# Kernel tuning notes

Hardware: AMD Instinct MI355X
Metric: run time of the kernel (lower is better)

Reference implementation:

```python
import jax, jax.numpy as jnp
import numpy as np

HID = 32
R = 3
B = 2
IN = 64
N = 100000
E = 1600000
G = 256


def setup_inputs() -> dict:
    key = jax.random.key(0)
    ks = jax.random.split(key, 16)
    x = jax.random.normal(ks[0], (N, IN), dtype=jnp.float32)
    src = jax.random.randint(ks[1], (E,), 0, N)
    dst = jax.random.randint(ks[2], (E,), 0, N)
    etype = jax.random.randint(ks[3], (E,), 0, R)
    graph_ids = jnp.sort(jax.random.randint(ks[4], (N,), 0, G))
    s = 0.05
    basis1 = jax.random.normal(ks[5], (B, IN, HID), dtype=jnp.float32) * s   # layer 1 basis
    basis_r = jax.random.normal(ks[6], (3, B, HID, HID), dtype=jnp.float32) * s  # layers 2-4
    w_comp = jax.random.normal(ks[7], (4, R, B), dtype=jnp.float32) * s     # per-layer basis coeffs
    loop1 = jax.random.normal(ks[8], (IN, HID), dtype=jnp.float32) * s
    loop_r = jax.random.normal(ks[9], (3, HID, HID), dtype=jnp.float32) * s
    bias = jnp.zeros((4, HID), dtype=jnp.float32)
    lin1_w = jax.random.normal(ks[10], (4 * HID, 64), dtype=jnp.float32) * s
    lin1_b = jnp.zeros((64,), dtype=jnp.float32)
    lin2_w = jax.random.normal(ks[11], (64, 1), dtype=jnp.float32) * s
    lin2_b = jnp.zeros((1,), dtype=jnp.float32)
    return dict(x=x, basis1=basis1, basis_r=basis_r, w_comp=w_comp, loop1=loop1,
                loop_r=loop_r, bias=bias, lin1_w=lin1_w, lin1_b=lin1_b,
                lin2_w=lin2_w, lin2_b=lin2_b, src=src, dst=dst, etype=etype,
                graph_ids=graph_ids, num_graphs=G)


def _rel_conv(h, basis, comp, loop_w, b, src, dst, etype, n_nodes):
    # basis-decomposed relation weights: W[r] = sum_b comp[r,b] * basis[b]
    W = jnp.einsum('rb,bio->rio', comp, basis)            # [R, in, out]
    h_rel = jnp.einsum('ni,rio->rno', h, W)               # [R, N, out]
    msg = h_rel[etype, src]                               # [E, out] edge-typed gather
    agg = jax.ops.segment_sum(msg, dst, num_segments=n_nodes)
    return agg + h @ loop_w + b                           # self-loop + bias


def reference(x, basis1, basis_r, w_comp, loop1, loop_r, bias,
              lin1_w, lin1_b, lin2_w, lin2_b,
              src, dst, etype, graph_ids, num_graphs):
    n = x.shape[0]
    h = jnp.tanh(_rel_conv(x, basis1, w_comp[0], loop1, bias[0], src, dst, etype, n))
    states = [h]
    for i in range(3):
        h = jnp.tanh(_rel_conv(h, basis_r[i], w_comp[i + 1], loop_r[i], bias[i + 1],
                               src, dst, etype, n))
        states.append(h)
    feat = jnp.concatenate(states, axis=1)                # [N, 128]
    # mean-pool nodes per graph (diff_pooling ~ dgl mean_nodes)
    summed = jax.ops.segment_sum(feat, graph_ids, num_segments=num_graphs)
    counts = jax.ops.segment_sum(jnp.ones((n,), feat.dtype), graph_ids,
                                 num_segments=num_graphs)
    pooled = summed / jnp.maximum(counts, 1.0)[:, None]   # [G, 128]
    hdn = jax.nn.relu(pooled @ lin1_w + lin1_b)
    out = jax.nn.sigmoid(hdn @ lin2_w + lin2_b)
    return out[:, 0]
```

## Files before the change

### kernel.cpp

```cpp
#include <hip/hip_runtime.h>
#include <cstdint>
#include <cmath>

#define DLO_BITS 7
#define DLO_MASK 127

__global__ __launch_bounds__(256) void prep_w1(
    const float* __restrict__ basis1,
    const float* __restrict__ w_comp,
    float* __restrict__ W1)
{
    int tid = blockIdx.x * 256 + threadIdx.x;
    if (tid < 6144) {
        int r = tid / 2048, io = tid % 2048;
        W1[tid] = w_comp[r*2] * basis1[io] + w_comp[r*2+1] * basis1[2048 + io];
    }
}

__global__ __launch_bounds__(256) void count_kernel(
    const int* __restrict__ dst, int* __restrict__ bcnt, int E, int NB)
{
    __shared__ int cnt[1024];
    for (int i = threadIdx.x; i < NB; i += 256) cnt[i] = 0;
    __syncthreads();
    int base = blockIdx.x * 4096;
    #pragma unroll
    for (int i = 0; i < 16; ++i) {
        int e = base + i * 256 + threadIdx.x;
        if (e < E) atomicAdd(&cnt[dst[e] >> DLO_BITS], 1);
    }
    __syncthreads();
    for (int i = threadIdx.x; i < NB; i += 256)
        if (cnt[i]) atomicAdd(&bcnt[i], cnt[i]);
}

__global__ __launch_bounds__(1024) void scan_kernel(
    const int* __restrict__ bcnt, int* __restrict__ bbase,
    int* __restrict__ bcur, int NB)
{
    __shared__ int s[1024];
    int t = threadIdx.x;
    int v = (t < NB) ? bcnt[t] : 0;
    s[t] = v; __syncthreads();
    for (int off = 1; off < 1024; off <<= 1) {
        int u = (t >= off) ? s[t - off] : 0;
        __syncthreads();
        s[t] += u;
        __syncthreads();
    }
    if (t < NB) { int b = s[t] - v; bbase[t] = b; bcur[t] = b; }
}

__global__ __launch_bounds__(256) void bscatter_kernel(
    const int* __restrict__ src, const int* __restrict__ dst,
    const int* __restrict__ et, int* __restrict__ bcur,
    unsigned* __restrict__ eidx1, int E, int NB)
{
    __shared__ int cnt[1024];
    __shared__ int bbs[1024];
    int tid = threadIdx.x;
    for (int i = tid; i < NB; i += 256) cnt[i] = 0;
    __syncthreads();
    int base = blockIdx.x * 8192;
    int lim = E - base; if (lim > 8192) lim = 8192;
    for (int i = tid; i < lim; i += 256)
        atomicAdd(&cnt[dst[base + i] >> DLO_BITS], 1);
    __syncthreads();
    for (int i = tid; i < NB; i += 256) {
        int c = cnt[i];
        bbs[i] = c ? atomicAdd(&bcur[i], c) : 0;
    }
    __syncthreads();
    for (int i = tid; i < NB; i += 256) cnt[i] = 0;
    __syncthreads();
    for (int i = tid; i < lim; i += 256) {
        int e = base + i;
        int d = dst[e];
        int bk = d >> DLO_BITS;
        int p = bbs[bk] + atomicAdd(&cnt[bk], 1);
        eidx1[p] = (unsigned)src[e] | ((unsigned)et[e] << 17)
                 | ((unsigned)(d & DLO_MASK) << 19);
    }
}

__global__ __launch_bounds__(256) void bucket_sort_kernel(
    const unsigned* __restrict__ eidx1, const int* __restrict__ bbase,
    const int* __restrict__ bcnt, unsigned* __restrict__ eidx2,
    int* __restrict__ row_ptr, int* __restrict__ deg, int N)
{
    __shared__ int c128[128], excl[128], w[128];
    int tid = threadIdx.x, b = blockIdx.x;
    int gbase = bbase[b], cnt = bcnt[b], n0 = b << DLO_BITS;
    if (tid < 128) c128[tid] = 0;
    __syncthreads();
    for (int k = tid; k < cnt; k += 256)
        atomicAdd(&c128[(eidx1[gbase + k] >> 19) & DLO_MASK], 1);
    __syncthreads();
    if (tid < 128) w[tid] = c128[tid];
    __syncthreads();
    for (int off = 1; off < 128; off <<= 1) {
        int u = (tid < 128 && tid >= off) ? w[tid - off] : 0;
        __syncthreads();
        if (tid < 128) w[tid] += u;
        __syncthreads();
    }
    if (tid < 128) {
        excl[tid] = w[tid] - c128[tid];
        int n = n0 + tid;
        if (n < N) { row_ptr[n] = gbase + excl[tid]; deg[n] = c128[tid]; }
        c128[tid] = 0;
    }
    __syncthreads();
    for (int k = tid; k < cnt; k += 256) {
        unsigned pk = eidx1[gbase + k];
        int dlo = (pk >> 19) & DLO_MASK;
        int p = excl[dlo] + atomicAdd(&c128[dlo], 1);
        eidx2[gbase + p] = pk;
    }
}

__global__ __launch_bounds__(256) void dense_kernel(
    const float* __restrict__ x,
    const float* __restrict__ Wrel,
    const float* __restrict__ Wloop,
    const float* __restrict__ bias_l,
    float* __restrict__ hrel,
    float* __restrict__ agg,
    int N)
{
    __shared__ float sW[4 * 2048];
    __shared__ float sH[64 * 68];
    const int tid = threadIdx.x;
    for (int i = tid; i < 3 * 2048; i += 256) sW[i] = Wrel[i];
    for (int i = tid; i < 2048; i += 256) sW[6144 + i] = Wloop[i];
    const int nb = blockIdx.x * 64;
    for (int idx = tid; idx < 64 * 64; idx += 256) {
        int n = idx >> 6, i = idx & 63;
        int gn = nb + n;
        sH[n * 68 + i] = (gn < N) ? x[(size_t)gn * 64 + i] : 0.0f;
    }
    __syncthreads();

    const int m  = tid >> 6;
    const int l  = tid & 63;
    const int ow = l & 7;
    const int ng = l >> 3;

    float acc[8][4];
    #pragma unroll
    for (int j = 0; j < 8; ++j)
        #pragma unroll
        for (int k = 0; k < 4; ++k) acc[j][k] = 0.0f;

    const float* wb = &sW[m * 2048 + ow * 4];
    #pragma unroll 2
    for (int i = 0; i < 64; i += 4) {
        float4 wv0 = *(const float4*)(wb + (i + 0) * 32);
        float4 wv1 = *(const float4*)(wb + (i + 1) * 32);
        float4 wv2 = *(const float4*)(wb + (i + 2) * 32);
        float4 wv3 = *(const float4*)(wb + (i + 3) * 32);
        #pragma unroll
        for (int j = 0; j < 8; ++j) {
            float4 hv = *(const float4*)&sH[(j * 8 + ng) * 68 + i];
            acc[j][0] += hv.x * wv0.x + hv.y * wv1.x + hv.z * wv2.x + hv.w * wv3.x;
            acc[j][1] += hv.x * wv0.y + hv.y * wv1.y + hv.z * wv2.y + hv.w * wv3.y;
            acc[j][2] += hv.x * wv0.z + hv.y * wv1.z + hv.z * wv2.z + hv.w * wv3.z;
            acc[j][3] += hv.x * wv0.w + hv.y * wv1.w + hv.z * wv2.w + hv.w * wv3.w;
        }
    }

    if (m < 3) {
        #pragma unroll
        for (int j = 0; j < 8; ++j) {
            int n = nb + j * 8 + ng;
            if (n < N)
                *(float4*)&hrel[((size_t)m * N + n) * 32 + ow * 4] =
                    make_float4(acc[j][0], acc[j][1], acc[j][2], acc[j][3]);
        }
    } else {
        float4 bb = *(const float4*)&bias_l[ow * 4];
        #pragma unroll
        for (int j = 0; j < 8; ++j) {
            int n = nb + j * 8 + ng;
            if (n < N)
                *(float4*)&agg[(size_t)n * 32 + ow * 4] =
                    make_float4(acc[j][0] + bb.x, acc[j][1] + bb.y,
                                acc[j][2] + bb.z, acc[j][3] + bb.w);
        }
    }
}

__global__ __launch_bounds__(256) void gather1_kernel(
    const unsigned* __restrict__ eidx, const int* __restrict__ row_ptr,
    const int* __restrict__ deg, const float* __restrict__ hrel,
    const float* __restrict__ agg, float* __restrict__ feat, int N)
{
    int tid = blockIdx.x * 256 + threadIdx.x;
    int n = tid >> 3;
    if (n >= N) return;
    int c = (tid & 7) << 2;
    int base = row_ptr[n], cnt = deg[n];
    const float4 bv = *(const float4*)&agg[(size_t)n * 32 + c];
    float a0[4] = {bv.x, bv.y, bv.z, bv.w};
    float a1[4] = {0, 0, 0, 0}, a2[4] = {0, 0, 0, 0}, a3[4] = {0, 0, 0, 0};
    int k = 0;
    for (; k + 4 <= cnt; k += 4) {
        unsigned p0 = eidx[base + k + 0], p1 = eidx[base + k + 1];
        unsigned p2 = eidx[base + k + 2], p3 = eidx[base + k + 3];
        float4 v0 = *(const float4*)&hrel[(((size_t)((p0 >> 17) & 3)) * N + (p0 & 0x1FFFF)) * 32 + c];
        float4 v1 = *(const float4*)&hrel[(((size_t)((p1 >> 17) & 3)) * N + (p1 & 0x1FFFF)) * 32 + c];
        float4 v2 = *(const float4*)&hrel[(((size_t)((p2 >> 17) & 3)) * N + (p2 & 0x1FFFF)) * 32 + c];
        float4 v3 = *(const float4*)&hrel[(((size_t)((p3 >> 17) & 3)) * N + (p3 & 0x1FFFF)) * 32 + c];
        a0[0] += v0.x; a0[1] += v0.y; a0[2] += v0.z; a0[3] += v0.w;
        a1[0] += v1.x; a1[1] += v1.y; a1[2] += v1.z; a1[3] += v1.w;
        a2[0] += v2.x; a2[1] += v2.y; a2[2] += v2.z; a2[3] += v2.w;
        a3[0] += v3.x; a3[1] += v3.y; a3[2] += v3.z; a3[3] += v3.w;
    }
    for (; k < cnt; ++k) {
        unsigned p = eidx[base + k];
        float4 v = *(const float4*)&hrel[(((size_t)((p >> 17) & 3)) * N + (p & 0x1FFFF)) * 32 + c];
        a0[0] += v.x; a0[1] += v.y; a0[2] += v.z; a0[3] += v.w;
    }
    float r0 = a0[0] + a1[0] + a2[0] + a3[0];
    float r1 = a0[1] + a1[1] + a2[1] + a3[1];
    float r2 = a0[2] + a1[2] + a2[2] + a3[2];
    float r3 = a0[3] + a1[3] + a2[3] + a3[3];
    float4* out = (float4*)&feat[(size_t)n * 128 + c];
    *out = make_float4(tanhf(r0), tanhf(r1), tanhf(r2), tanhf(r3));
}

__global__ __launch_bounds__(256) void fused_layer_kernel(
    const unsigned* __restrict__ eidx, const int* __restrict__ row_ptr,
    const int* __restrict__ deg,
    const float* __restrict__ basis_b,
    const float* __restrict__ loop_w,
    const float* __restrict__ bias_l,
    const float* __restrict__ comp,
    const float* __restrict__ feat_in,
    float* __restrict__ feat_out,
    int N)
{
    __shared__ float sB0[1024], sB1[1024], sL[1024];
    __shared__ float sT0[32 * 36], sT1[32 * 36], sH[32 * 36];
    const int tid = threadIdx.x;
    for (int i = tid; i < 1024; i += 256) {
        sB0[i] = basis_b[i];
        sB1[i] = basis_b[1024 + i];
        sL[i]  = loop_w[i];
    }
    const float cc0r0 = comp[0], cc1r0 = comp[1];
    const float cc0r1 = comp[2], cc1r1 = comp[3];
    const float cc0r2 = comp[4], cc1r2 = comp[5];

    const int nn = tid >> 3, cg = (tid & 7) << 2;
    const int n = blockIdx.x * 32 + nn;

    float4 h4 = *(const float4*)&feat_in[(size_t)n * 128 + cg];
    *(float4*)&sH[nn * 36 + cg] = h4;

    const int base = row_ptr[n], cnt = deg[n];
    float t0a[4] = {0,0,0,0}, t1a[4] = {0,0,0,0};
    float t0b[4] = {0,0,0,0}, t1b[4] = {0,0,0,0};
    int k = 0;
    for (; k + 4 <= cnt; k += 4) {
        unsigned p0 = eidx[base + k + 0], p1 = eidx[base + k + 1];
        unsigned p2 = eidx[base + k + 2], p3 = eidx[base + k + 3];
        int r0 = (p0 >> 17) & 3, r1 = (p1 >> 17) & 3;
        int r2 = (p2 >> 17) & 3, r3 = (p3 >> 17) & 3;
        float4 v0 = *(const float4*)&feat_in[(size_t)(p0 & 0x1FFFF) * 128 + cg];
        float4 v1 = *(const float4*)&feat_in[(size_t)(p1 & 0x1FFFF) * 128 + cg];
        float4 v2 = *(const float4*)&feat_in[(size_t)(p2 & 0x1FFFF) * 128 + cg];
        float4 v3 = *(const float4*)&feat_in[(size_t)(p3 & 0x1FFFF) * 128 + cg];
        float c00 = r0 == 0 ? cc0r0 : (r0 == 1 ? cc0r1 : cc0r2);
        float c10 = r0 == 0 ? cc1r0 : (r0 == 1 ? cc1r1 : cc1r2);
        float c01 = r1 == 0 ? cc0r0 : (r1 == 1 ? cc0r1 : cc0r2);
        float c11 = r1 == 0 ? cc1r0 : (r1 == 1 ? cc1r1 : cc1r2);
        float c02 = r2 == 0 ? cc0r0 : (r2 == 1 ? cc0r1 : cc0r2);
        float c12 = r2 == 0 ? cc1r0 : (r2 == 1 ? cc1r1 : cc1r2);
        float c03 = r3 == 0 ? cc0r0 : (r3 == 1 ? cc0r1 : cc0r2);
        float c13 = r3 == 0 ? cc1r0 : (r3 == 1 ? cc1r1 : cc1r2);
        t0a[0] += c00*v0.x; t0a[1] += c00*v0.y; t0a[2] += c00*v0.z; t0a[3] += c00*v0.w;
        t1a[0] += c10*v0.x; t1a[1] += c10*v0.y; t1a[2] += c10*v0.z; t1a[3] += c10*v0.w;
        t0b[0] += c01*v1.x; t0b[1] += c01*v1.y; t0b[2] += c01*v1.z; t0b[3] += c01*v1.w;
        t1b[0] += c11*v1.x; t1b[1] += c11*v1.y; t1b[2] += c11*v1.z; t1b[3] += c11*v1.w;
        t0a[0] += c02*v2.x; t0a[1] += c02*v2.y; t0a[2] += c02*v2.z; t0a[3] += c02*v2.w;
        t1a[0] += c12*v2.x; t1a[1] += c12*v2.y; t1a[2] += c12*v2.z; t1a[3] += c12*v2.w;
        t0b[0] += c03*v3.x; t0b[1] += c03*v3.y; t0b[2] += c03*v3.z; t0b[3] += c03*v3.w;
        t1b[0] += c13*v3.x; t1b[1] += c13*v3.y; t1b[2] += c13*v3.z; t1b[3] += c13*v3.w;
    }
    for (; k < cnt; ++k) {
        unsigned p = eidx[base + k];
        int r = (p >> 17) & 3;
        float4 v = *(const float4*)&feat_in[(size_t)(p & 0x1FFFF) * 128 + cg];
        float c0 = r == 0 ? cc0r0 : (r == 1 ? cc0r1 : cc0r2);
        float c1 = r == 0 ? cc1r0 : (r == 1 ? cc1r1 : cc1r2);
        t0a[0] += c0*v.x; t0a[1] += c0*v.y; t0a[2] += c0*v.z; t0a[3] += c0*v.w;
        t1a[0] += c1*v.x; t1a[1] += c1*v.y; t1a[2] += c1*v.z; t1a[3] += c1*v.w;
    }
    *(float4*)&sT0[nn * 36 + cg] = make_float4(t0a[0]+t0b[0], t0a[1]+t0b[1],
                                               t0a[2]+t0b[2], t0a[3]+t0b[3]);
    *(float4*)&sT1[nn * 36 + cg] = make_float4(t1a[0]+t1b[0], t1a[1]+t1b[1],
                                               t1a[2]+t1b[2], t1a[3]+t1b[3]);
    __syncthreads();

    float4 bb = *(const float4*)&bias_l[cg];
    float a[4] = {bb.x, bb.y, bb.z, bb.w};
    #pragma unroll 8
    for (int kk = 0; kk < 32; ++kk) {
        float p0 = sT0[nn * 36 + kk];
        float p1 = sT1[nn * 36 + kk];
        float hh = sH[nn * 36 + kk];
        float4 b0 = *(const float4*)&sB0[kk * 32 + cg];
        float4 b1 = *(const float4*)&sB1[kk * 32 + cg];
        float4 lw = *(const float4*)&sL[kk * 32 + cg];
        a[0] += p0 * b0.x + p1 * b1.x + hh * lw.x;
        a[1] += p0 * b0.y + p1 * b1.y + hh * lw.y;
        a[2] += p0 * b0.z + p1 * b1.z + hh * lw.z;
        a[3] += p0 * b0.w + p1 * b1.w + hh * lw.w;
    }
    *(float4*)&feat_out[(size_t)n * 128 + cg] =
        make_float4(tanhf(a[0]), tanhf(a[1]), tanhf(a[2]), tanhf(a[3]));
}

__global__ __launch_bounds__(256) void pool_kernel(
    const float* __restrict__ feat, const int* __restrict__ gid,
    float* __restrict__ pooled, float* __restrict__ cntArr, int N)
{
    int chunk0 = blockIdx.x * 128;
    int ch = threadIdx.x & 127, half = threadIdx.x >> 7;
    int n = chunk0 + half;
    int lim = chunk0 + 128; if (lim > N) lim = N;
    if (n >= lim) return;
    int cur = gid[n];
    float acc = 0.0f; int cc = 0;
    for (; n < lim; n += 2) {
        int g = gid[n];
        if (g != cur) {
            atomicAdd(&pooled[(size_t)cur * 128 + ch], acc);
            if (ch == 0) atomicAdd(&cntArr[cur], (float)cc);
            acc = 0.0f; cc = 0; cur = g;
        }
        acc += feat[(size_t)n * 128 + ch];
        ++cc;
    }
    atomicAdd(&pooled[(size_t)cur * 128 + ch], acc);
    if (ch == 0) atomicAdd(&cntArr[cur], (float)cc);
}

__global__ __launch_bounds__(64) void mlp_kernel(
    const float* __restrict__ pooled, const float* __restrict__ cntArr,
    const float* __restrict__ w1, const float* __restrict__ b1,
    const float* __restrict__ w2, const float* __restrict__ b2,
    float* __restrict__ out)
{
    int g = blockIdx.x;
    int t = threadIdx.x;
    float inv = 1.0f / fmaxf(cntArr[g], 1.0f);
    float acc = b1[t];
    #pragma unroll 8
    for (int k = 0; k < 128; ++k)
        acc += pooled[(size_t)g * 128 + k] * inv * w1[k * 64 + t];
    float h = fmaxf(acc, 0.0f);
    float p = h * w2[t];
    #pragma unroll
    for (int off = 32; off > 0; off >>= 1) p += __shfl_down(p, off, 64);
    if (t == 0) out[g] = 1.0f / (1.0f + expf(-(p + b2[0])));
}

extern "C" void kernel_launch(void* const* d_in, const int* in_sizes, int n_in,
                              void* d_out, int out_size, void* d_ws, size_t ws_size,
                              hipStream_t stream)
{
    const float* x       = (const float*)d_in[0];
    const float* basis1  = (const float*)d_in[1];
    const float* basis_r = (const float*)d_in[2];
    const float* w_comp  = (const float*)d_in[3];
    const float* loop1   = (const float*)d_in[4];
    const float* loop_r  = (const float*)d_in[5];
    const float* bias    = (const float*)d_in[6];
    const float* lin1_w  = (const float*)d_in[7];
    const float* lin1_b  = (const float*)d_in[8];
    const float* lin2_w  = (const float*)d_in[9];
    const float* lin2_b  = (const float*)d_in[10];
    const int*   src     = (const int*)d_in[11];
    const int*   dst     = (const int*)d_in[12];
    const int*   etype   = (const int*)d_in[13];
    const int*   gid     = (const int*)d_in[14];

    const int N = in_sizes[0] / 64;
    const int E = in_sizes[11];
    const int G = out_size;
    const int NB = (N + DLO_MASK) >> DLO_BITS;

    float* ws      = (float*)d_ws;
    float* W1      = ws;
    float* hrel    = W1 + 6144;
    float* agg     = hrel + (size_t)3 * N * 32;
    float* feat    = agg + (size_t)N * 32;
    float* pooled  = feat + (size_t)N * 128;
    float* cntArr  = pooled + (size_t)G * 128;
    int*   bcnt    = (int*)(cntArr + G);
    int*   bbase   = bcnt + NB;
    int*   bcur    = bbase + NB;
    int*   row_ptr = bcur + NB;
    int*   deg     = row_ptr + N;
    unsigned* eidx2 = (unsigned*)(deg + N);
    unsigned* eidx1 = (unsigned*)feat;

    hipMemsetAsync(pooled, 0, ((size_t)G * 128 + G + NB) * sizeof(float), stream);
    prep_w1<<<24, 256, 0, stream>>>(basis1, w_comp, W1);

    count_kernel<<<(E + 4095) / 4096, 256, 0, stream>>>(dst, bcnt, E, NB);
    scan_kernel<<<1, 1024, 0, stream>>>(bcnt, bbase, bcur, NB);
    bscatter_kernel<<<(E + 8191) / 8192, 256, 0, stream>>>(src, dst, etype, bcur, eidx1, E, NB);
    bucket_sort_kernel<<<NB, 256, 0, stream>>>(eidx1, bbase, bcnt, eidx2, row_ptr, deg, N);

    dense_kernel<<<(N + 63) / 64, 256, 0, stream>>>(x, W1, loop1, bias, hrel, agg, N);
    gather1_kernel<<<(N * 8 + 255) / 256, 256, 0, stream>>>(eidx2, row_ptr, deg, hrel, agg, feat, N);

    for (int l = 1; l < 4; ++l) {
        fused_layer_kernel<<<(N + 31) / 32, 256, 0, stream>>>(
            eidx2, row_ptr, deg,
            basis_r + (size_t)(l - 1) * 2048,
            loop_r + (size_t)(l - 1) * 1024,
            bias + l * 32,
            w_comp + l * 6,
            feat + (l - 1) * 32,
            feat + l * 32,
            N);
    }

    pool_kernel<<<NB, 256, 0, stream>>>(feat, gid, pooled, cntArr, N);
    mlp_kernel<<<G, 64, 0, stream>>>(pooled, cntArr, lin1_w, lin1_b, lin2_w, lin2_b, (float*)d_out);
}
```

Baseline: 313.6 us.

## Replace two-level bucket sort CSR build with global atomic counting sort

Replaces the bucketed two-pass CSR construction (block histogram, bucket scatter, per-bucket local sort) with a per-node degree count using global atomics, a three-kernel multi-block prefix scan, and a direct atomic scatter into final edge positions. Row end is derived from the post-scatter cursor, so degree storage is dropped. It also folds the layer-1 basis combination into the dense kernel and reads x directly from global memory instead of staging it in shared memory. The atomic scatter gives a nondeterministic edge order within each row and puts heavy contention on global atomics, and the scattered writes lose the locality the bucket pass provided.

Measured after the change: 471.1 us. 50.2% more time.

```diff
diff --git a/kernel.cpp b/kernel.cpp
--- a/kernel.cpp
+++ b/kernel.cpp
@@ -2,45 +2,31 @@
 #include <cstdint>
 #include <cmath>
 
-#define DLO_BITS 7
-#define DLO_MASK 127
-
-__global__ __launch_bounds__(256) void prep_w1(
-    const float* __restrict__ basis1,
-    const float* __restrict__ w_comp,
-    float* __restrict__ W1)
+
+__global__ __launch_bounds__(256) void deg_count_kernel(
+    const int* __restrict__ dst, int* __restrict__ deg, int E)
 {
     int tid = blockIdx.x * 256 + threadIdx.x;
-    if (tid < 6144) {
-        int r = tid / 2048, io = tid % 2048;
-        W1[tid] = w_comp[r*2] * basis1[io] + w_comp[r*2+1] * basis1[2048 + io];
-    }
-}
-
-__global__ __launch_bounds__(256) void count_kernel(
-    const int* __restrict__ dst, int* __restrict__ bcnt, int E, int NB)
-{
-    __shared__ int cnt[1024];
-    for (int i = threadIdx.x; i < NB; i += 256) cnt[i] = 0;
-    __syncthreads();
-    int base = blockIdx.x * 4096;
-    #pragma unroll
-    for (int i = 0; i < 16; ++i) {
-        int e = base + i * 256 + threadIdx.x;
-        if (e < E) atomicAdd(&cnt[dst[e] >> DLO_BITS], 1);
-    }
-    __syncthreads();
-    for (int i = threadIdx.x; i < NB; i += 256)
-        if (cnt[i]) atomicAdd(&bcnt[i], cnt[i]);
-}
-
-__global__ __launch_bounds__(1024) void scan_kernel(
-    const int* __restrict__ bcnt, int* __restrict__ bbase,
-    int* __restrict__ bcur, int NB)
+    int e0 = tid * 4;
+    if (e0 + 4 <= E) {
+        int4 d = ((const int4*)dst)[tid];
+        atomicAdd(&deg[d.x], 1);
+        atomicAdd(&deg[d.y], 1);
+        atomicAdd(&deg[d.z], 1);
+        atomicAdd(&deg[d.w], 1);
+    } else {
+        for (int e = e0; e < E; ++e) atomicAdd(&deg[dst[e]], 1);
+    }
+}
+
+__global__ __launch_bounds__(1024) void scan1_kernel(
+    const int* __restrict__ deg, int* __restrict__ rp,
+    int* __restrict__ bsum, int N)
 {
     __shared__ int s[1024];
     int t = threadIdx.x;
-    int v = (t < NB) ? bcnt[t] : 0;
+    int n = blockIdx.x * 1024 + t;
+    int v = (n < N) ? deg[n] : 0;
     s[t] = v; __syncthreads();
     for (int off = 1; off < 1024; off <<= 1) {
         int u = (t >= off) ? s[t - off] : 0;
@@ -48,96 +34,78 @@
         s[t] += u;
         __syncthreads();
     }
-    if (t < NB) { int b = s[t] - v; bbase[t] = b; bcur[t] = b; }
-}
-
-__global__ __launch_bounds__(256) void bscatter_kernel(
+    if (n < N) rp[n] = s[t] - v;
+    if (t == 1023) bsum[blockIdx.x] = s[1023];
+}
+
+__global__ __launch_bounds__(128) void scan2_kernel(int* __restrict__ bsum, int NS)
+{
+    __shared__ int s[128];
+    int t = threadIdx.x;
+    int v = (t < NS) ? bsum[t] : 0;
+    s[t] = v; __syncthreads();
+    for (int off = 1; off < 128; off <<= 1) {
+        int u = (t >= off) ? s[t - off] : 0;
+        __syncthreads();
+        s[t] += u;
+        __syncthreads();
+    }
+    if (t < NS) bsum[t] = s[t] - v;
+}
+
+__global__ __launch_bounds__(256) void scan3_kernel(
+    int* __restrict__ rp, int* __restrict__ cur, const int* __restrict__ bsum, int N)
+{
+    int n = blockIdx.x * 256 + threadIdx.x;
+    if (n < N) {
+        int b = rp[n] + bsum[n >> 10];
+        rp[n] = b;
+        cur[n] = b;
+    }
+}
+
+__global__ __launch_bounds__(256) void scatter_kernel(
     const int* __restrict__ src, const int* __restrict__ dst,
-    const int* __restrict__ et, int* __restrict__ bcur,
-    unsigned* __restrict__ eidx1, int E, int NB)
-{
-    __shared__ int cnt[1024];
-    __shared__ int bbs[1024];
-    int tid = threadIdx.x;
-    for (int i = tid; i < NB; i += 256) cnt[i] = 0;
-    __syncthreads();
-    int base = blockIdx.x * 8192;
-    int lim = E - base; if (lim > 8192) lim = 8192;
-    for (int i = tid; i < lim; i += 256)
-        atomicAdd(&cnt[dst[base + i] >> DLO_BITS], 1);
-    __syncthreads();
-    for (int i = tid; i < NB; i += 256) {
-        int c = cnt[i];
-        bbs[i] = c ? atomicAdd(&bcur[i], c) : 0;
-    }
-    __syncthreads();
-    for (int i = tid; i < NB; i += 256) cnt[i] = 0;
-    __syncthreads();
-    for (int i = tid; i < lim; i += 256) {
-        int e = base + i;
-        int d = dst[e];
-        int bk = d >> DLO_BITS;
-        int p = bbs[bk] + atomicAdd(&cnt[bk], 1);
-        eidx1[p] = (unsigned)src[e] | ((unsigned)et[e] << 17)
-                 | ((unsigned)(d & DLO_MASK) << 19);
-    }
-}
-
-__global__ __launch_bounds__(256) void bucket_sort_kernel(
-    const unsigned* __restrict__ eidx1, const int* __restrict__ bbase,
-    const int* __restrict__ bcnt, unsigned* __restrict__ eidx2,
-    int* __restrict__ row_ptr, int* __restrict__ deg, int N)
-{
-    __shared__ int c128[128], excl[128], w[128];
-    int tid = threadIdx.x, b = blockIdx.x;
-    int gbase = bbase[b], cnt = bcnt[b], n0 = b << DLO_BITS;
-    if (tid < 128) c128[tid] = 0;
-    __syncthreads();
-    for (int k = tid; k < cnt; k += 256)
-        atomicAdd(&c128[(eidx1[gbase + k] >> 19) & DLO_MASK], 1);
-    __syncthreads();
-    if (tid < 128) w[tid] = c128[tid];
-    __syncthreads();
-    for (int off = 1; off < 128; off <<= 1) {
-        int u = (tid < 128 && tid >= off) ? w[tid - off] : 0;
-        __syncthreads();
-        if (tid < 128) w[tid] += u;
-        __syncthreads();
-    }
-    if (tid < 128) {
-        excl[tid] = w[tid] - c128[tid];
-        int n = n0 + tid;
-        if (n < N) { row_ptr[n] = gbase + excl[tid]; deg[n] = c128[tid]; }
-        c128[tid] = 0;
-    }
-    __syncthreads();
-    for (int k = tid; k < cnt; k += 256) {
-        unsigned pk = eidx1[gbase + k];
-        int dlo = (pk >> 19) & DLO_MASK;
-        int p = excl[dlo] + atomicAdd(&c128[dlo], 1);
-        eidx2[gbase + p] = pk;
-    }
-}
-
-__global__ __launch_bounds__(256) void dense_kernel(
+    const int* __restrict__ et, int* __restrict__ cur,
+    unsigned* __restrict__ eidx, int E)
+{
+    int tid = blockIdx.x * 256 + threadIdx.x;
+    int e0 = tid * 4;
+    if (e0 + 4 <= E) {
+        int4 s4 = ((const int4*)src)[tid];
+        int4 d4 = ((const int4*)dst)[tid];
+        int4 t4 = ((const int4*)et)[tid];
+        int p;
+        p = atomicAdd(&cur[d4.x], 1); eidx[p] = (unsigned)s4.x | ((unsigned)t4.x << 17);
+        p = atomicAdd(&cur[d4.y], 1); eidx[p] = (unsigned)s4.y | ((unsigned)t4.y << 17);
+        p = atomicAdd(&cur[d4.z], 1); eidx[p] = (unsigned)s4.z | ((unsigned)t4.z << 17);
+        p = atomicAdd(&cur[d4.w], 1); eidx[p] = (unsigned)s4.w | ((unsigned)t4.w << 17);
+    } else {
+        for (int e = e0; e < E; ++e) {
+            int p = atomicAdd(&cur[dst[e]], 1);
+            eidx[p] = (unsigned)src[e] | ((unsigned)et[e] << 17);
+        }
+    }
+}
+
+__global__ __launch_bounds__(256, 4) void dense_kernel(
     const float* __restrict__ x,
-    const float* __restrict__ Wrel,
-    const float* __restrict__ Wloop,
+    const float* __restrict__ basis1,
+    const float* __restrict__ loop1,
+    const float* __restrict__ w_comp,
     const float* __restrict__ bias_l,
     float* __restrict__ hrel,
     float* __restrict__ agg,
     int N)
 {
     __shared__ float sW[4 * 2048];
-    __shared__ float sH[64 * 68];
     const int tid = threadIdx.x;
-    for (int i = tid; i < 3 * 2048; i += 256) sW[i] = Wrel[i];
-    for (int i = tid; i < 2048; i += 256) sW[6144 + i] = Wloop[i];
-    const int nb = blockIdx.x * 64;
-    for (int idx = tid; idx < 64 * 64; idx += 256) {
-        int n = idx >> 6, i = idx & 63;
-        int gn = nb + n;
-        sH[n * 68 + i] = (gn < N) ? x[(size_t)gn * 64 + i] : 0.0f;
+    for (int i = tid; i < 4 * 2048; i += 256) {
+        int m = i >> 11, io = i & 2047;
+        float v;
+        if (m < 3) v = w_comp[m * 2] * basis1[io] + w_comp[m * 2 + 1] * basis1[2048 + io];
+        else       v = loop1[io];
+        sW[i] = v;
     }
     __syncthreads();
 
@@ -145,6 +113,15 @@
     const int l  = tid & 63;
     const int ow = l & 7;
     const int ng = l >> 3;
+    const int nb = blockIdx.x * 64;
+
+    const float* xr[8];
+    #pragma unroll
+    for (int j = 0; j < 8; ++j) {
+        int gn = nb + j * 8 + ng;
+        if (gn > N - 1) gn = N - 1;
+        xr[j] = x + (size_t)gn * 64;
+    }
 
     float acc[8][4];
     #pragma unroll
@@ -161,7 +138,7 @@
         float4 wv3 = *(const float4*)(wb + (i + 3) * 32);
         #pragma unroll
         for (int j = 0; j < 8; ++j) {
-            float4 hv = *(const float4*)&sH[(j * 8 + ng) * 68 + i];
+            float4 hv = *(const float4*)(xr[j] + i);
             acc[j][0] += hv.x * wv0.x + hv.y * wv1.x + hv.z * wv2.x + hv.w * wv3.x;
             acc[j][1] += hv.x * wv0.y + hv.y * wv1.y + hv.z * wv2.y + hv.w * wv3.y;
             acc[j][2] += hv.x * wv0.z + hv.y * wv1.z + hv.z * wv2.z + hv.w * wv3.z;
@@ -191,15 +168,15 @@
 }
 
 __global__ __launch_bounds__(256) void gather1_kernel(
-    const unsigned* __restrict__ eidx, const int* __restrict__ row_ptr,
-    const int* __restrict__ deg, const float* __restrict__ hrel,
+    const unsigned* __restrict__ eidx, const int* __restrict__ rp,
+    const int* __restrict__ rend, const float* __restrict__ hrel,
     const float* __restrict__ agg, float* __restrict__ feat, int N)
 {
     int tid = blockIdx.x * 256 + threadIdx.x;
     int n = tid >> 3;
     if (n >= N) return;
     int c = (tid & 7) << 2;
-    int base = row_ptr[n], cnt = deg[n];
+    int base = rp[n], cnt = rend[n] - base;
     const float4 bv = *(const float4*)&agg[(size_t)n * 32 + c];
     float a0[4] = {bv.x, bv.y, bv.z, bv.w};
     float a1[4] = {0, 0, 0, 0}, a2[4] = {0, 0, 0, 0}, a3[4] = {0, 0, 0, 0};
@@ -230,8 +207,8 @@
 }
 
 __global__ __launch_bounds__(256) void fused_layer_kernel(
-    const unsigned* __restrict__ eidx, const int* __restrict__ row_ptr,
-    const int* __restrict__ deg,
+    const unsigned* __restrict__ eidx, const int* __restrict__ rp,
+    const int* __restrict__ rend,
     const float* __restrict__ basis_b,
     const float* __restrict__ loop_w,
     const float* __restrict__ bias_l,
@@ -258,7 +235,7 @@
     float4 h4 = *(const float4*)&feat_in[(size_t)n * 128 + cg];
     *(float4*)&sH[nn * 36 + cg] = h4;
 
-    const int base = row_ptr[n], cnt = deg[n];
+    const int base = rp[n], cnt = rend[n] - base;
     float t0a[4] = {0,0,0,0}, t1a[4] = {0,0,0,0};
     float t0b[4] = {0,0,0,0}, t1b[4] = {0,0,0,0};
     int k = 0;
@@ -390,37 +367,33 @@
     const int N = in_sizes[0] / 64;
     const int E = in_sizes[11];
     const int G = out_size;
-    const int NB = (N + DLO_MASK) >> DLO_BITS;
+    const int NSB = (N + 1023) >> 10;
 
     float* ws      = (float*)d_ws;
-    float* W1      = ws;
-    float* hrel    = W1 + 6144;
+    float* hrel    = ws;
     float* agg     = hrel + (size_t)3 * N * 32;
     float* feat    = agg + (size_t)N * 32;
     float* pooled  = feat + (size_t)N * 128;
     float* cntArr  = pooled + (size_t)G * 128;
-    int*   bcnt    = (int*)(cntArr + G);
-    int*   bbase   = bcnt + NB;
-    int*   bcur    = bbase + NB;
-    int*   row_ptr = bcur + NB;
-    int*   deg     = row_ptr + N;
-    unsigned* eidx2 = (unsigned*)(deg + N);
-    unsigned* eidx1 = (unsigned*)feat;
-
-    hipMemsetAsync(pooled, 0, ((size_t)G * 128 + G + NB) * sizeof(float), stream);
-    prep_w1<<<24, 256, 0, stream>>>(basis1, w_comp, W1);
-
-    count_kernel<<<(E + 4095) / 4096, 256, 0, stream>>>(dst, bcnt, E, NB);
-    scan_kernel<<<1, 1024, 0, stream>>>(bcnt, bbase, bcur, NB);
-    bscatter_kernel<<<(E + 8191) / 8192, 256, 0, stream>>>(src, dst, etype, bcur, eidx1, E, NB);
-    bucket_sort_kernel<<<NB, 256, 0, stream>>>(eidx1, bbase, bcnt, eidx2, row_ptr, deg, N);
-
-    dense_kernel<<<(N + 63) / 64, 256, 0, stream>>>(x, W1, loop1, bias, hrel, agg, N);
-    gather1_kernel<<<(N * 8 + 255) / 256, 256, 0, stream>>>(eidx2, row_ptr, deg, hrel, agg, feat, N);
+    int*   rend    = (int*)(cntArr + G);
+    int*   rp      = rend + N;
+    int*   bsum    = rp + N;
+    unsigned* eidx2 = (unsigned*)(bsum + 128);
+
+    hipMemsetAsync(pooled, 0, ((size_t)G * 128 + G + N) * sizeof(float), stream);
+
+    deg_count_kernel<<<(E / 4 + 255) / 256, 256, 0, stream>>>(dst, rend, E);
+    scan1_kernel<<<NSB, 1024, 0, stream>>>(rend, rp, bsum, N);
+    scan2_kernel<<<1, 128, 0, stream>>>(bsum, NSB);
+    scan3_kernel<<<(N + 255) / 256, 256, 0, stream>>>(rp, rend, bsum, N);
+    scatter_kernel<<<(E / 4 + 255) / 256, 256, 0, stream>>>(src, dst, etype, rend, eidx2, E);
+
+    dense_kernel<<<(N + 63) / 64, 256, 0, stream>>>(x, basis1, loop1, w_comp, bias, hrel, agg, N);
+    gather1_kernel<<<(N * 8 + 255) / 256, 256, 0, stream>>>(eidx2, rp, rend, hrel, agg, feat, N);
 
     for (int l = 1; l < 4; ++l) {
         fused_layer_kernel<<<(N + 31) / 32, 256, 0, stream>>>(
-            eidx2, row_ptr, deg,
+            eidx2, rp, rend,
             basis_r + (size_t)(l - 1) * 2048,
             loop_r + (size_t)(l - 1) * 1024,
             bias + l * 32,
@@ -430,6 +403,6 @@
             N);
     }
 
-    pool_kernel<<<NB, 256, 0, stream>>>(feat, gid, pooled, cntArr, N);
+    pool_kernel<<<(N + 127) / 128, 256, 0, stream>>>(feat, gid, pooled, cntArr, N);
     mlp_kernel<<<G, 64, 0, stream>>>(pooled, cntArr, lin1_w, lin1_b, lin2_w, lin2_b, (float*)d_out);
 }
```
